# Kernel tuning notes

Measured on AMD Instinct MI355X. Metric: run time of the kernel, lower is better.

Reference implementation:

```python
import jax
import jax.numpy as jnp
import numpy as np

B, T, D = 4, 2048, 2048
H, HS = 32, 64
E5, TD = 5 * 32, 64
LAYER_ID, NUM_LAYERS = 12, 24


def setup_inputs() -> dict:
    key = jax.random.key(0)
    ks = jax.random.split(key, 12)
    r01 = LAYER_ID / max(NUM_LAYERS - 1, 1)          # ratio_0_to_1
    r1a0 = 1.0 - LAYER_ID / NUM_LAYERS               # ratio_1_to_almost0
    ddd = np.arange(D, dtype=np.float32) / D
    i = np.arange(D, dtype=np.float32)
    decay = (-6.0 + 5.0 * (i / max(D - 1, 1)) ** (0.7 + 1.3 * r01)).reshape(H, HS)
    first = (r01 * (1.0 - i / max(D - 1, 1)) + ((i + 1) % 3 - 1) * 0.1).reshape(H, HS)
    s = 1.0 / np.sqrt(D)
    inp = {
        "x": jax.random.normal(ks[0], (B, T, D), jnp.float32),
        "prev": jax.random.normal(ks[1], (B, D), jnp.float32),
        "state": jnp.zeros((B, H, HS, HS), jnp.float32),
        "x_maa": jnp.asarray(1.0 - ddd ** r1a0),
        "w_maa": jnp.asarray(1.0 - ddd ** r1a0),
        "k_maa": jnp.asarray(1.0 - ddd ** r1a0),
        "v_maa": jnp.asarray(1.0 - (ddd ** r1a0 + 0.3 * r01)),
        "r_maa": jnp.asarray(1.0 - ddd ** (0.5 * r1a0)),
        "g_maa": jnp.asarray(1.0 - ddd ** (0.5 * r1a0)),
        "tm_w1": jax.random.normal(ks[2], (D, E5), jnp.float32) * 0.01,
        "tm_w2": jax.random.normal(ks[3], (5, E5 // 5, D), jnp.float32) * 0.01,
        "td_w1": jax.random.normal(ks[4], (D, TD), jnp.float32) * 0.01,
        "td_w2": jax.random.normal(ks[5], (TD, D), jnp.float32) * 0.01,
        "time_decay": jnp.asarray(decay),
        "time_first": jnp.asarray(first),
        "W_r": jax.random.normal(ks[6], (D, D), jnp.float32) * s,
        "W_k": jax.random.normal(ks[7], (D, D), jnp.float32) * s,
        "W_v": jax.random.normal(ks[8], (D, D), jnp.float32) * s,
        "W_g": jax.random.normal(ks[9], (D, D), jnp.float32) * s,
        "W_o": jax.random.normal(ks[10], (D, D), jnp.float32) * s,
        "ln_g": jnp.ones((D,), jnp.float32),
        "ln_b": jnp.zeros((D,), jnp.float32),
    }
    return inp


def _wkv(r, k, v, w, u, state):
    # r,k,v,w: [T,B,H,HS]; u: [H,HS]; state: [B,H,K,V]
    ub = u[None, :, :, None]  # broadcast over batch and value dim

    def step(st, inp):
        rt, kt, vt, wt = inp                      # [B,H,HS]
        kv = kt[..., :, None] * vt[..., None, :]  # [B,H,K,V]
        out = jnp.einsum('bhk,bhkv->bhv', rt, st + ub * kv)
        st = st * wt[..., :, None] + kv
        return st, out

    new_state, outs = jax.lax.scan(step, state, (r, k, v, w))
    return outs, new_state  # outs: [T,B,H,HS]


def reference(x, prev, state, x_maa, w_maa, k_maa, v_maa, r_maa, g_maa,
              tm_w1, tm_w2, td_w1, td_w2, time_decay, time_first,
              W_r, W_k, W_v, W_g, W_o, ln_g, ln_b):
    B_, T_, D_ = x.shape
    H_, HS_ = time_decay.shape
    shifted = jnp.concatenate([prev[:, None, :], x[:, :-1]], axis=1)
    sx = shifted - x
    xxx = x + sx * x_maa
    m = jnp.tanh(xxx @ tm_w1).reshape(B_, T_, 5, -1)
    mix = jnp.einsum('btfe,fed->fbtd', m, tm_w2)  # [5,B,T,D]
    mw, mk, mv, mr, mg = mix
    wx = x + sx * (w_maa + mw)
    kx = x + sx * (k_maa + mk)
    vx = x + sx * (v_maa + mv)
    rx = x + sx * (r_maa + mr)
    gx = x + sx * (g_maa + mg)
    r = jax.nn.sigmoid(rx @ W_r)
    k = kx @ W_k
    v = vx @ W_v
    g = jax.nn.silu(gx @ W_g)
    w = jnp.tanh(wx @ td_w1) @ td_w2
    w = w.reshape(B_, T_, H_, HS_) + time_decay  # broadcast [H,HS]
    w = jnp.exp(-jnp.exp(w))

    def to_tbhd(a):
        return a.reshape(B_, T_, H_, HS_).transpose(1, 0, 2, 3)

    outs, new_state = _wkv(to_tbhd(r), to_tbhd(k), to_tbhd(v),
                           to_tbhd(w), time_first, state)
    out = outs.transpose(1, 0, 2, 3).reshape(B_ * T_, H_, HS_)
    mu = out.mean(-1, keepdims=True)
    var = out.var(-1, keepdims=True)
    out = ((out - mu) / jnp.sqrt(var + 1e-5)).reshape(B_ * T_, D_)
    out = (out * ln_g + ln_b).reshape(B_, T_, D_)
    out = (out * g) @ W_o
    return out, x[:, -1], new_state
```

## Files before the change

kernel.cpp:

```cpp
#include <hip/hip_runtime.h>
#include <stdint.h>

typedef unsigned short u16;
typedef __attribute__((ext_vector_type(8))) short s16x8;
typedef __attribute__((ext_vector_type(4))) float f32x4;

#define DEVFN static __device__ __forceinline__

constexpr int BB = 4, TT = 2048, DD = 2048, HH = 32;
constexpr int MM = BB * TT;
constexpr size_t MD = (size_t)MM * DD;
constexpr int CC = 128, NC = 16;

DEVFN u16 f2b(float f) {
  unsigned int b = __float_as_uint(f);
  unsigned int r = (b + 0x7fffu + ((b >> 16) & 1u)) >> 16;
  return (u16)r;
}
DEVFN float b2f(u16 u) { return __uint_as_float(((unsigned int)u) << 16); }
DEVFN ushort4 pack4(float4 v) {
  ushort4 o; o.x = f2b(v.x); o.y = f2b(v.y); o.z = f2b(v.z); o.w = f2b(v.w); return o;
}

DEVFN void gload16(const void* g, void* l) {
  __builtin_amdgcn_global_load_lds(
      (const __attribute__((address_space(1))) unsigned int*)g,
      (__attribute__((address_space(3))) unsigned int*)l, 16, 0, 0);
}

__global__ __launch_bounds__(256) void k_xxx(
    const float* __restrict__ x, const float* __restrict__ prev,
    const float* __restrict__ xmaa, u16* __restrict__ xxxb,
    float* __restrict__ xlast) {
  size_t e = ((size_t)blockIdx.x * 256 + threadIdx.x) * 4;
  int d = (int)(e % DD);
  int m = (int)(e / DD);
  int b = m >> 11, t = m & (TT - 1);
  float4 xv = *(const float4*)(x + e);
  float4 sh = (t == 0) ? *(const float4*)(prev + (size_t)b * DD + d)
                       : *(const float4*)(x + e - DD);
  float4 xm = *(const float4*)(xmaa + d);
  float4 xx = make_float4(xv.x + (sh.x - xv.x) * xm.x, xv.y + (sh.y - xv.y) * xm.y,
                          xv.z + (sh.z - xv.z) * xm.z, xv.w + (sh.w - xv.w) * xm.w);
  *(ushort4*)(xxxb + e) = pack4(xx);
  if (t == TT - 1) *(float4*)(xlast + (size_t)b * DD + d) = xv;
}

__global__ __launch_bounds__(256) void k_transpose(
    const float* __restrict__ src, u16* __restrict__ dst,
    int K, int N, int Kpad, int Npad) {
  __shared__ float tile[64][65];
  int k0 = blockIdx.x * 64, n0 = blockIdx.y * 64;
  int tid = threadIdx.x;
#pragma unroll
  for (int it = 0; it < 16; ++it) {
    int flat = it * 256 + tid;
    int r = flat >> 6, c = flat & 63;
    int kk = k0 + r, nn = n0 + c;
    tile[r][c] = (kk < K && nn < N) ? src[(size_t)kk * N + nn] : 0.f;
  }
  __syncthreads();
#pragma unroll
  for (int it = 0; it < 16; ++it) {
    int flat = it * 256 + tid;
    int r = flat >> 6, c = flat & 63;
    dst[(size_t)(n0 + r) * Kpad + (k0 + c)] = f2b(tile[c][r]);
  }
}

__global__ __launch_bounds__(256) void k_tmw1(const float* __restrict__ src,
                                              u16* __restrict__ dst) {
  int idx = blockIdx.x * 256 + threadIdx.x;
  int n = idx >> 11, kk = idx & 2047;
  int f = n >> 6, c = n & 63;
  float v = (f < 5 && c < 32) ? src[(size_t)kk * 160 + f * 32 + c] : 0.f;
  dst[idx] = f2b(v);
}

__global__ __launch_bounds__(256) void gemm_bt(
    const u16* __restrict__ A, int lda, const u16* __restrict__ Bt, int ldb,
    void* __restrict__ Out, int ldc, int K, int mode,
    const float* __restrict__ colvec, const float* __restrict__ xf32,
    const float* __restrict__ prevf32) {
  __shared__ u16 As[128 * 64];
  __shared__ u16 Bs[128 * 64];
  const int tid = threadIdx.x;
  const int m0 = blockIdx.x * 128, n0 = blockIdx.y * 128;
  const int wv = tid >> 6, lane = tid & 63;
  const int wr = wv >> 1, wc = wv & 1;
  const int lrow = lane & 15, kgrp = lane >> 4;
  const int srow = lane >> 3;
  const int scol = (lane & 7) * 8;
  f32x4 acc[4][4];
#pragma unroll
  for (int i = 0; i < 4; i++)
#pragma unroll
    for (int j = 0; j < 4; j++) acc[i][j] = {0.f, 0.f, 0.f, 0.f};

  for (int k0 = 0; k0 < K; k0 += 64) {
#pragma unroll
    for (int it = 0; it < 4; ++it) {
      int rbase = it * 32 + wv * 8;
      gload16(A + (size_t)(m0 + rbase + srow) * lda + k0 + scol, &As[rbase * 64]);
      gload16(Bt + (size_t)(n0 + rbase + srow) * ldb + k0 + scol, &Bs[rbase * 64]);
    }
    __syncthreads();
#pragma unroll
    for (int ks = 0; ks < 64; ks += 32) {
      s16x8 af[4], bfr[4];
#pragma unroll
      for (int mi = 0; mi < 4; mi++)
        af[mi] = *(const s16x8*)(&As[(wr * 64 + mi * 16 + lrow) * 64 + ks + kgrp * 8]);
#pragma unroll
      for (int ni = 0; ni < 4; ni++)
        bfr[ni] = *(const s16x8*)(&Bs[(wc * 64 + ni * 16 + lrow) * 64 + ks + kgrp * 8]);
#pragma unroll
      for (int mi = 0; mi < 4; mi++)
#pragma unroll
        for (int ni = 0; ni < 4; ni++)
          acc[mi][ni] = __builtin_amdgcn_mfma_f32_16x16x32_bf16(af[mi], bfr[ni],
                                                                acc[mi][ni], 0, 0, 0);
    }
    __syncthreads();
  }
#pragma unroll
  for (int mi = 0; mi < 4; mi++) {
#pragma unroll
    for (int ni = 0; ni < 4; ni++) {
      int row0 = m0 + wr * 64 + mi * 16 + kgrp * 4;
      int col = n0 + wc * 64 + ni * 16 + lrow;
#pragma unroll
      for (int q = 0; q < 4; q++) {
        int row = row0 + q;
        size_t o = (size_t)row * ldc + col;
        float v = acc[mi][ni][q];
        if (mode == 0) {
          ((u16*)Out)[o] = f2b(v);
        } else if (mode == 1) {
          ((u16*)Out)[o] = f2b(1.f / (1.f + __expf(-v)));
        } else if (mode == 2) {
          ((u16*)Out)[o] = f2b(v / (1.f + __expf(-v)));
        } else if (mode == 3) {
          ((u16*)Out)[o] = f2b(tanhf(v));
        } else if (mode == 4) {
          ((float*)Out)[o] = __expf(-__expf(v + colvec[col]));
        } else if (mode == 5) {
          int b = row >> 11, t = row & (TT - 1);
          size_t xo = (size_t)row * DD + col;
          float xv = xf32[xo];
          float sh = (t == 0) ? prevf32[(size_t)b * DD + col] : xf32[xo - DD];
          ((u16*)Out)[o] = f2b(xv + (sh - xv) * (colvec[col] + v));
        } else {
          ((float*)Out)[o] = v;
        }
      }
    }
  }
}


__global__ __launch_bounds__(64) void k_scan1(
    const u16* __restrict__ k, const u16* __restrict__ v,
    const float* __restrict__ w, float* __restrict__ L, float* __restrict__ P) {
  int idx = blockIdx.x;
  int bh = idx / NC, c = idx % NC;
  int b = bh >> 5, h = bh & 31;
  int j = threadIdx.x;
  float4 s[16];
#pragma unroll
  for (int i = 0; i < 16; i++) s[i] = make_float4(0.f, 0.f, 0.f, 0.f);
  float pj = 1.f;
  __shared__ __align__(16) float ks[64];
  __shared__ __align__(16) float wsd[64];
  size_t base = ((size_t)b * TT + (size_t)c * CC) * DD + h * 64 + j;
  float kc = b2f(k[base]), vc = b2f(v[base]), wc = w[base];
  for (int t = 0; t < CC; ++t) {
    ks[j] = kc; wsd[j] = wc;
    float vg = vc, wcur = wc;
    __syncthreads();
    size_t nb = base + DD;
    if (t + 1 < CC) { kc = b2f(k[nb]); vc = b2f(v[nb]); wc = w[nb]; }
    pj *= wcur;
#pragma unroll
    for (int i = 0; i < 16; i++) {
      float4 k4 = *(const float4*)(ks + i * 4);
      float4 w4 = *(const float4*)(wsd + i * 4);
      float4 s4 = s[i];
      s4.x = fmaf(s4.x, w4.x, k4.x * vg);
      s4.y = fmaf(s4.y, w4.y, k4.y * vg);
      s4.z = fmaf(s4.z, w4.z, k4.z * vg);
      s4.w = fmaf(s4.w, w4.w, k4.w * vg);
      s[i] = s4;
    }
    base = nb;
    __syncthreads();
  }
  float* Lp = L + (size_t)idx * 4096;
#pragma unroll
  for (int i = 0; i < 16; i++) {
    Lp[(i * 4 + 0) * 64 + j] = s[i].x;
    Lp[(i * 4 + 1) * 64 + j] = s[i].y;
    Lp[(i * 4 + 2) * 64 + j] = s[i].z;
    Lp[(i * 4 + 3) * 64 + j] = s[i].w;
  }
  P[(size_t)idx * 64 + j] = pj;
}

__global__ __launch_bounds__(64) void k_scan2(
    float* LS, const float* __restrict__ P, const float* __restrict__ st_in) {
  int bh = blockIdx.x;
  int j = threadIdx.x;
  const float* si = st_in + (size_t)bh * 4096;
  float4 s[16];
#pragma unroll
  for (int i = 0; i < 16; i++) {
    s[i].x = si[(i * 4 + 0) * 64 + j];
    s[i].y = si[(i * 4 + 1) * 64 + j];
    s[i].z = si[(i * 4 + 2) * 64 + j];
    s[i].w = si[(i * 4 + 3) * 64 + j];
  }
  for (int c = 0; c < NC; ++c) {
    size_t slot = ((size_t)bh * NC + c) * 4096;
    if (c > 0) {
      float* dst = LS + ((size_t)bh * NC + c - 1) * 4096;
#pragma unroll
      for (int i = 0; i < 16; i++) {
        dst[(i * 4 + 0) * 64 + j] = s[i].x;
        dst[(i * 4 + 1) * 64 + j] = s[i].y;
        dst[(i * 4 + 2) * 64 + j] = s[i].z;
        dst[(i * 4 + 3) * 64 + j] = s[i].w;
      }
    }
    const float* Pc = P + ((size_t)bh * NC + c) * 64;
#pragma unroll
    for (int i = 0; i < 16; i++) {
      float4 p4 = *(const float4*)(Pc + i * 4);
      float lx = LS[slot + (i * 4 + 0) * 64 + j];
      float ly = LS[slot + (i * 4 + 1) * 64 + j];
      float lz = LS[slot + (i * 4 + 2) * 64 + j];
      float lw = LS[slot + (i * 4 + 3) * 64 + j];
      s[i].x = fmaf(s[i].x, p4.x, lx);
      s[i].y = fmaf(s[i].y, p4.y, ly);
      s[i].z = fmaf(s[i].z, p4.z, lz);
      s[i].w = fmaf(s[i].w, p4.w, lw);
    }
  }
}

__global__ __launch_bounds__(64) void k_scan3(
    const u16* __restrict__ r, const u16* __restrict__ k,
    const u16* __restrict__ v, const float* __restrict__ w,
    const float* __restrict__ u, const float* __restrict__ st_in,
    const float* __restrict__ LS, u16* __restrict__ wkv,
    float* __restrict__ st_out) {
  int idx = blockIdx.x;
  int bh = idx / NC, c = idx % NC;
  int b = bh >> 5, h = bh & 31;
  int j = threadIdx.x;
  const float* sp = (c == 0) ? st_in + (size_t)bh * 4096
                             : LS + ((size_t)bh * NC + c - 1) * 4096;
  float4 s[16];
#pragma unroll
  for (int i = 0; i < 16; i++) {
    s[i].x = sp[(i * 4 + 0) * 64 + j];
    s[i].y = sp[(i * 4 + 1) * 64 + j];
    s[i].z = sp[(i * 4 + 2) * 64 + j];
    s[i].w = sp[(i * 4 + 3) * 64 + j];
  }
  float4 uu[16];
  const float* up = u + h * 64;
#pragma unroll
  for (int i = 0; i < 16; i++) uu[i] = *(const float4*)(up + i * 4);
  __shared__ __align__(16) float rs[64];
  __shared__ __align__(16) float ks[64];
  __shared__ __align__(16) float wsd[64];
  size_t base = ((size_t)b * TT + (size_t)c * CC) * DD + h * 64 + j;
  float rc = b2f(r[base]), kc = b2f(k[base]), vc = b2f(v[base]), wc = w[base];
  for (int t = 0; t < CC; ++t) {
    rs[j] = rc; ks[j] = kc; wsd[j] = wc;
    float vg = vc;
    __syncthreads();
    size_t nb = base + DD;
    if (t + 1 < CC) { rc = b2f(r[nb]); kc = b2f(k[nb]); vc = b2f(v[nb]); wc = w[nb]; }
    float acc = 0.f;
#pragma unroll
    for (int i = 0; i < 16; i++) {
      float4 r4 = *(const float4*)(rs + i * 4);
      float4 k4 = *(const float4*)(ks + i * 4);
      float4 w4 = *(const float4*)(wsd + i * 4);
      float4 u4 = uu[i];
      float4 s4 = s[i];
      float kv;
      kv = k4.x * vg; acc += r4.x * fmaf(u4.x, kv, s4.x); s4.x = fmaf(s4.x, w4.x, kv);
      kv = k4.y * vg; acc += r4.y * fmaf(u4.y, kv, s4.y); s4.y = fmaf(s4.y, w4.y, kv);
      kv = k4.z * vg; acc += r4.z * fmaf(u4.z, kv, s4.z); s4.z = fmaf(s4.z, w4.z, kv);
      kv = k4.w * vg; acc += r4.w * fmaf(u4.w, kv, s4.w); s4.w = fmaf(s4.w, w4.w, kv);
      s[i] = s4;
    }
    wkv[base] = f2b(acc);
    base = nb;
    __syncthreads();
  }
  if (c == NC - 1) {
    float* so = st_out + (size_t)bh * 4096;
#pragma unroll
    for (int i = 0; i < 16; i++) {
      so[(i * 4 + 0) * 64 + j] = s[i].x;
      so[(i * 4 + 1) * 64 + j] = s[i].y;
      so[(i * 4 + 2) * 64 + j] = s[i].z;
      so[(i * 4 + 3) * 64 + j] = s[i].w;
    }
  }
}

__global__ __launch_bounds__(256) void k_gnorm(
    const u16* __restrict__ wkv, const u16* __restrict__ g,
    const float* __restrict__ lng, const float* __restrict__ lnb,
    u16* __restrict__ outg) {
  int gi = blockIdx.x * 4 + (threadIdx.x >> 6);
  int lane = threadIdx.x & 63;
  int row = gi >> 5, h = gi & 31;
  size_t o = (size_t)row * DD + h * 64 + lane;
  float val = b2f(wkv[o]);
  float s1 = val, s2 = val * val;
#pragma unroll
  for (int off = 32; off; off >>= 1) {
    s1 += __shfl_xor(s1, off);
    s2 += __shfl_xor(s2, off);
  }
  float mu = s1 * (1.f / 64.f);
  float var = s2 * (1.f / 64.f) - mu * mu;
  float nv = (val - mu) * rsqrtf(var + 1e-5f);
  int d = h * 64 + lane;
  float ov = (nv * lng[d] + lnb[d]) * b2f(g[o]);
  outg[o] = f2b(ov);
}

extern "C" void kernel_launch(void* const* d_in, const int* in_sizes, int n_in,
                              void* d_out, int out_size, void* d_ws, size_t ws_size,
                              hipStream_t stream) {
  const float* x = (const float*)d_in[0];
  const float* prev = (const float*)d_in[1];
  const float* st = (const float*)d_in[2];
  const float* x_maa = (const float*)d_in[3];
  const float* w_maa = (const float*)d_in[4];
  const float* k_maa = (const float*)d_in[5];
  const float* v_maa = (const float*)d_in[6];
  const float* r_maa = (const float*)d_in[7];
  const float* g_maa = (const float*)d_in[8];
  const float* tm_w1 = (const float*)d_in[9];
  const float* tm_w2 = (const float*)d_in[10];
  const float* td_w1 = (const float*)d_in[11];
  const float* td_w2 = (const float*)d_in[12];
  const float* decay = (const float*)d_in[13];
  const float* first = (const float*)d_in[14];
  const float* W_r = (const float*)d_in[15];
  const float* W_k = (const float*)d_in[16];
  const float* W_v = (const float*)d_in[17];
  const float* W_g = (const float*)d_in[18];
  const float* W_o = (const float*)d_in[19];
  const float* ln_g = (const float*)d_in[20];
  const float* ln_b = (const float*)d_in[21];

  float* out = (float*)d_out;
  float* xlast = out + MD;
  float* stout = xlast + (size_t)BB * DD;
  float* wf32 = out;

  char* p = (char*)d_ws;
  const size_t SLOT = MD * 2;
  u16* slotA = (u16*)p; p += SLOT;
  u16* slotB = (u16*)p; p += SLOT;
  u16* slotC = (u16*)p; p += SLOT;
  u16* slotD = (u16*)p; p += SLOT;
  u16* slotE = (u16*)p; p += SLOT;
  u16* mbuf = (u16*)p; p += (size_t)MM * 384 * 2;
  u16* hbuf = (u16*)p; p += (size_t)MM * 128 * 2;
  u16* Wrt = (u16*)p; p += (size_t)DD * DD * 2;
  u16* Wkt = (u16*)p; p += (size_t)DD * DD * 2;
  u16* Wvt = (u16*)p; p += (size_t)DD * DD * 2;
  u16* Wgt = (u16*)p; p += (size_t)DD * DD * 2;
  u16* Wot = (u16*)p; p += (size_t)DD * DD * 2;
  u16* tmw1t = (u16*)p; p += (size_t)384 * 2048 * 2;
  u16* w2t = (u16*)p; p += (size_t)5 * 2048 * 64 * 2;
  u16* tdw1t = (u16*)p; p += (size_t)128 * 2048 * 2;
  u16* tdw2t = (u16*)p; p += (size_t)2048 * 128 * 2;

  float* LS = (float*)Wrt;
  float* Pbuf = (float*)hbuf;

  dim3 b256(256);
  k_transpose<<<dim3(32, 32), b256, 0, stream>>>(W_r, Wrt, 2048, 2048, 2048, 2048);
  k_transpose<<<dim3(32, 32), b256, 0, stream>>>(W_k, Wkt, 2048, 2048, 2048, 2048);
  k_transpose<<<dim3(32, 32), b256, 0, stream>>>(W_v, Wvt, 2048, 2048, 2048, 2048);
  k_transpose<<<dim3(32, 32), b256, 0, stream>>>(W_g, Wgt, 2048, 2048, 2048, 2048);
  k_transpose<<<dim3(32, 32), b256, 0, stream>>>(W_o, Wot, 2048, 2048, 2048, 2048);
  k_transpose<<<dim3(32, 2), b256, 0, stream>>>(td_w1, tdw1t, 2048, 64, 2048, 128);
  k_transpose<<<dim3(2, 32), b256, 0, stream>>>(td_w2, tdw2t, 64, 2048, 128, 2048);
  for (int f = 0; f < 5; ++f)
    k_transpose<<<dim3(1, 32), b256, 0, stream>>>(
        tm_w2 + (size_t)f * 32 * 2048, w2t + (size_t)f * 2048 * 64, 32, 2048, 64, 2048);
  k_tmw1<<<3072, b256, 0, stream>>>(tm_w1, tmw1t);

  k_xxx<<<(int)(MD / 4 / 256), b256, 0, stream>>>(x, prev, x_maa, slotA, xlast);

  gemm_bt<<<dim3(MM / 128, 3), b256, 0, stream>>>(slotA, 2048, tmw1t, 2048, mbuf, 384,
                                                  2048, 3, nullptr, nullptr, nullptr);

  const float* maas[5] = {w_maa, k_maa, v_maa, r_maa, g_maa};
  gemm_bt<<<dim3(MM / 128, 16), b256, 0, stream>>>(mbuf + 3 * 64, 384, w2t + (size_t)3 * 2048 * 64,
                                                   64, slotB, 2048, 64, 5, maas[3], x, prev);
  gemm_bt<<<dim3(MM / 128, 16), b256, 0, stream>>>(slotB, 2048, Wrt, 2048, slotA, 2048,
                                                   2048, 1, nullptr, nullptr, nullptr);
  gemm_bt<<<dim3(MM / 128, 16), b256, 0, stream>>>(mbuf + 1 * 64, 384, w2t + (size_t)1 * 2048 * 64,
                                                   64, slotB, 2048, 64, 5, maas[1], x, prev);
  gemm_bt<<<dim3(MM / 128, 16), b256, 0, stream>>>(slotB, 2048, Wkt, 2048, slotC, 2048,
                                                   2048, 0, nullptr, nullptr, nullptr);
  gemm_bt<<<dim3(MM / 128, 16), b256, 0, stream>>>(mbuf + 2 * 64, 384, w2t + (size_t)2 * 2048 * 64,
                                                   64, slotB, 2048, 64, 5, maas[2], x, prev);
  gemm_bt<<<dim3(MM / 128, 16), b256, 0, stream>>>(slotB, 2048, Wvt, 2048, slotD, 2048,
                                                   2048, 0, nullptr, nullptr, nullptr);
  gemm_bt<<<dim3(MM / 128, 16), b256, 0, stream>>>(mbuf + 4 * 64, 384, w2t + (size_t)4 * 2048 * 64,
                                                   64, slotB, 2048, 64, 5, maas[4], x, prev);
  gemm_bt<<<dim3(MM / 128, 16), b256, 0, stream>>>(slotB, 2048, Wgt, 2048, slotE, 2048,
                                                   2048, 2, nullptr, nullptr, nullptr);
  gemm_bt<<<dim3(MM / 128, 16), b256, 0, stream>>>(mbuf + 0 * 64, 384, w2t + (size_t)0 * 2048 * 64,
                                                   64, slotB, 2048, 64, 5, maas[0], x, prev);
  gemm_bt<<<dim3(MM / 128, 1), b256, 0, stream>>>(slotB, 2048, tdw1t, 2048, hbuf, 128,
                                                  2048, 3, nullptr, nullptr, nullptr);
  gemm_bt<<<dim3(MM / 128, 16), b256, 0, stream>>>(hbuf, 128, tdw2t, 128, wf32, 2048,
                                                   128, 4, decay, nullptr, nullptr);

  k_scan1<<<BB * HH * NC, 64, 0, stream>>>(slotC, slotD, wf32, LS, Pbuf);
  k_scan2<<<BB * HH, 64, 0, stream>>>(LS, Pbuf, st);
  k_scan3<<<BB * HH * NC, 64, 0, stream>>>(slotA, slotC, slotD, wf32, first, st, LS,
                                           slotB, stout);

  k_gnorm<<<MM * HH / 4, b256, 0, stream>>>(slotB, slotE, ln_g, ln_b, slotA);

  gemm_bt<<<dim3(MM / 128, 16), b256, 0, stream>>>(slotA, 2048, Wot, 2048, out, 2048,
                                                   2048, 6, nullptr, nullptr, nullptr);
}
```

Measured before the change: 1.720 ms.

## Split mix epilogue into vectorized elementwise kernel and unroll scan loops by two

The lerp epilogue (mode 5) is removed from the GEMM. Each small mix GEMM now writes raw bf16 output, and a separate vectorized k_bx kernel applies x + sx*(maa + mix) in place. This replaces the scattered uncoalesced fp32 x/prev reads in the GEMM epilogue with float4 loads, at the cost of an extra kernel launch and an extra bf16 round trip per branch. Separately, k_scan1 and k_scan3 now process two timesteps per iteration, with double shared buffers and one barrier pair, halving synchronization. The extra rounding of the mix term to bf16 slightly changes numerics.

```diff
diff --git a/kernel.cpp b/kernel.cpp
--- a/kernel.cpp
+++ b/kernel.cpp
@@ -46,6 +46,26 @@
   if (t == TT - 1) *(float4*)(xlast + (size_t)b * DD + d) = xv;
 }
 
+__global__ __launch_bounds__(256) void k_bx(
+    const float* __restrict__ x, const float* __restrict__ prev,
+    const float* __restrict__ maa, u16* __restrict__ buf) {
+  size_t e = ((size_t)blockIdx.x * 256 + threadIdx.x) * 4;
+  int d = (int)(e % DD);
+  int m = (int)(e / DD);
+  int b = m >> 11, t = m & (TT - 1);
+  float4 xv = *(const float4*)(x + e);
+  float4 sh = (t == 0) ? *(const float4*)(prev + (size_t)b * DD + d)
+                       : *(const float4*)(x + e - DD);
+  float4 ma = *(const float4*)(maa + d);
+  ushort4 mu = *(const ushort4*)(buf + e);
+  float4 o;
+  o.x = xv.x + (sh.x - xv.x) * (ma.x + b2f(mu.x));
+  o.y = xv.y + (sh.y - xv.y) * (ma.y + b2f(mu.y));
+  o.z = xv.z + (sh.z - xv.z) * (ma.z + b2f(mu.z));
+  o.w = xv.w + (sh.w - xv.w) * (ma.w + b2f(mu.w));
+  *(ushort4*)(buf + e) = pack4(o);
+}
+
 __global__ __launch_bounds__(256) void k_transpose(
     const float* __restrict__ src, u16* __restrict__ dst,
     int K, int N, int Kpad, int Npad) {
@@ -80,8 +100,7 @@
 __global__ __launch_bounds__(256) void gemm_bt(
     const u16* __restrict__ A, int lda, const u16* __restrict__ Bt, int ldb,
     void* __restrict__ Out, int ldc, int K, int mode,
-    const float* __restrict__ colvec, const float* __restrict__ xf32,
-    const float* __restrict__ prevf32) {
+    const float* __restrict__ colvec) {
   __shared__ u16 As[128 * 64];
   __shared__ u16 Bs[128 * 64];
   const int tid = threadIdx.x;
@@ -144,12 +163,6 @@
           ((u16*)Out)[o] = f2b(tanhf(v));
         } else if (mode == 4) {
           ((float*)Out)[o] = __expf(-__expf(v + colvec[col]));
-        } else if (mode == 5) {
-          int b = row >> 11, t = row & (TT - 1);
-          size_t xo = (size_t)row * DD + col;
-          float xv = xf32[xo];
-          float sh = (t == 0) ? prevf32[(size_t)b * DD + col] : xf32[xo - DD];
-          ((u16*)Out)[o] = f2b(xv + (sh - xv) * (colvec[col] + v));
         } else {
           ((float*)Out)[o] = v;
         }
@@ -170,29 +183,34 @@
 #pragma unroll
   for (int i = 0; i < 16; i++) s[i] = make_float4(0.f, 0.f, 0.f, 0.f);
   float pj = 1.f;
-  __shared__ __align__(16) float ks[64];
-  __shared__ __align__(16) float wsd[64];
+  __shared__ __align__(16) float ks0[64], ws0[64], ks1[64], ws1[64];
   size_t base = ((size_t)b * TT + (size_t)c * CC) * DD + h * 64 + j;
-  float kc = b2f(k[base]), vc = b2f(v[base]), wc = w[base];
-  for (int t = 0; t < CC; ++t) {
-    ks[j] = kc; wsd[j] = wc;
-    float vg = vc, wcur = wc;
-    __syncthreads();
-    size_t nb = base + DD;
-    if (t + 1 < CC) { kc = b2f(k[nb]); vc = b2f(v[nb]); wc = w[nb]; }
-    pj *= wcur;
+  float kc0 = b2f(k[base]), vc0 = b2f(v[base]), wc0 = w[base];
+  float kc1 = b2f(k[base + DD]), vc1 = b2f(v[base + DD]), wc1 = w[base + DD];
+  for (int t = 0; t < CC; t += 2) {
+    ks0[j] = kc0; ws0[j] = wc0; ks1[j] = kc1; ws1[j] = wc1;
+    float vg0 = vc0, vg1 = vc1;
+    pj *= wc0 * wc1;
+    __syncthreads();
+    if (t + 2 < CC) {
+      size_t nb = base + 2 * DD;
+      kc0 = b2f(k[nb]); vc0 = b2f(v[nb]); wc0 = w[nb];
+      kc1 = b2f(k[nb + DD]); vc1 = b2f(v[nb + DD]); wc1 = w[nb + DD];
+    }
 #pragma unroll
     for (int i = 0; i < 16; i++) {
-      float4 k4 = *(const float4*)(ks + i * 4);
-      float4 w4 = *(const float4*)(wsd + i * 4);
+      float4 k40 = *(const float4*)(ks0 + i * 4);
+      float4 w40 = *(const float4*)(ws0 + i * 4);
+      float4 k41 = *(const float4*)(ks1 + i * 4);
+      float4 w41 = *(const float4*)(ws1 + i * 4);
       float4 s4 = s[i];
-      s4.x = fmaf(s4.x, w4.x, k4.x * vg);
-      s4.y = fmaf(s4.y, w4.y, k4.y * vg);
-      s4.z = fmaf(s4.z, w4.z, k4.z * vg);
-      s4.w = fmaf(s4.w, w4.w, k4.w * vg);
+      s4.x = fmaf(s4.x, w40.x, k40.x * vg0); s4.x = fmaf(s4.x, w41.x, k41.x * vg1);
+      s4.y = fmaf(s4.y, w40.y, k40.y * vg0); s4.y = fmaf(s4.y, w41.y, k41.y * vg1);
+      s4.z = fmaf(s4.z, w40.z, k40.z * vg0); s4.z = fmaf(s4.z, w41.z, k41.z * vg1);
+      s4.w = fmaf(s4.w, w40.w, k40.w * vg0); s4.w = fmaf(s4.w, w41.w, k41.w * vg1);
       s[i] = s4;
     }
-    base = nb;
+    base += 2 * DD;
     __syncthreads();
   }
   float* Lp = L + (size_t)idx * 4096;
@@ -271,34 +289,48 @@
   const float* up = u + h * 64;
 #pragma unroll
   for (int i = 0; i < 16; i++) uu[i] = *(const float4*)(up + i * 4);
-  __shared__ __align__(16) float rs[64];
-  __shared__ __align__(16) float ks[64];
-  __shared__ __align__(16) float wsd[64];
+  __shared__ __align__(16) float rs0[64], ks0[64], ws0[64];
+  __shared__ __align__(16) float rs1[64], ks1[64], ws1[64];
   size_t base = ((size_t)b * TT + (size_t)c * CC) * DD + h * 64 + j;
-  float rc = b2f(r[base]), kc = b2f(k[base]), vc = b2f(v[base]), wc = w[base];
-  for (int t = 0; t < CC; ++t) {
-    rs[j] = rc; ks[j] = kc; wsd[j] = wc;
-    float vg = vc;
-    __syncthreads();
-    size_t nb = base + DD;
-    if (t + 1 < CC) { rc = b2f(r[nb]); kc = b2f(k[nb]); vc = b2f(v[nb]); wc = w[nb]; }
-    float acc = 0.f;
+  float rc0 = b2f(r[base]), kc0 = b2f(k[base]), vc0 = b2f(v[base]), wc0 = w[base];
+  float rc1 = b2f(r[base + DD]), kc1 = b2f(k[base + DD]), vc1 = b2f(v[base + DD]),
+        wc1 = w[base + DD];
+  for (int t = 0; t < CC; t += 2) {
+    rs0[j] = rc0; ks0[j] = kc0; ws0[j] = wc0;
+    rs1[j] = rc1; ks1[j] = kc1; ws1[j] = wc1;
+    float vg0 = vc0, vg1 = vc1;
+    __syncthreads();
+    if (t + 2 < CC) {
+      size_t nb = base + 2 * DD;
+      rc0 = b2f(r[nb]); kc0 = b2f(k[nb]); vc0 = b2f(v[nb]); wc0 = w[nb];
+      rc1 = b2f(r[nb + DD]); kc1 = b2f(k[nb + DD]); vc1 = b2f(v[nb + DD]);
+      wc1 = w[nb + DD];
+    }
+    float acc0 = 0.f, acc1 = 0.f;
 #pragma unroll
     for (int i = 0; i < 16; i++) {
-      float4 r4 = *(const float4*)(rs + i * 4);
-      float4 k4 = *(const float4*)(ks + i * 4);
-      float4 w4 = *(const float4*)(wsd + i * 4);
+      float4 r40 = *(const float4*)(rs0 + i * 4);
+      float4 k40 = *(const float4*)(ks0 + i * 4);
+      float4 w40 = *(const float4*)(ws0 + i * 4);
+      float4 r41 = *(const float4*)(rs1 + i * 4);
+      float4 k41 = *(const float4*)(ks1 + i * 4);
+      float4 w41 = *(const float4*)(ws1 + i * 4);
       float4 u4 = uu[i];
       float4 s4 = s[i];
       float kv;
-      kv = k4.x * vg; acc += r4.x * fmaf(u4.x, kv, s4.x); s4.x = fmaf(s4.x, w4.x, kv);
-      kv = k4.y * vg; acc += r4.y * fmaf(u4.y, kv, s4.y); s4.y = fmaf(s4.y, w4.y, kv);
-      kv = k4.z * vg; acc += r4.z * fmaf(u4.z, kv, s4.z); s4.z = fmaf(s4.z, w4.z, kv);
-      kv = k4.w * vg; acc += r4.w * fmaf(u4.w, kv, s4.w); s4.w = fmaf(s4.w, w4.w, kv);
+      kv = k40.x * vg0; acc0 += r40.x * fmaf(u4.x, kv, s4.x); s4.x = fmaf(s4.x, w40.x, kv);
+      kv = k41.x * vg1; acc1 += r41.x * fmaf(u4.x, kv, s4.x); s4.x = fmaf(s4.x, w41.x, kv);
+      kv = k40.y * vg0; acc0 += r40.y * fmaf(u4.y, kv, s4.y); s4.y = fmaf(s4.y, w40.y, kv);
+      kv = k41.y * vg1; acc1 += r41.y * fmaf(u4.y, kv, s4.y); s4.y = fmaf(s4.y, w41.y, kv);
+      kv = k40.z * vg0; acc0 += r40.z * fmaf(u4.z, kv, s4.z); s4.z = fmaf(s4.z, w40.z, kv);
+      kv = k41.z * vg1; acc1 += r41.z * fmaf(u4.z, kv, s4.z); s4.z = fmaf(s4.z, w41.z, kv);
+      kv = k40.w * vg0; acc0 += r40.w * fmaf(u4.w, kv, s4.w); s4.w = fmaf(s4.w, w40.w, kv);
+      kv = k41.w * vg1; acc1 += r41.w * fmaf(u4.w, kv, s4.w); s4.w = fmaf(s4.w, w41.w, kv);
       s[i] = s4;
     }
-    wkv[base] = f2b(acc);
-    base = nb;
+    wkv[base] = f2b(acc0);
+    wkv[base + DD] = f2b(acc1);
+    base += 2 * DD;
     __syncthreads();
   }
   if (c == NC - 1) {
@@ -405,31 +437,42 @@
   k_xxx<<<(int)(MD / 4 / 256), b256, 0, stream>>>(x, prev, x_maa, slotA, xlast);
 
   gemm_bt<<<dim3(MM / 128, 3), b256, 0, stream>>>(slotA, 2048, tmw1t, 2048, mbuf, 384,
-                                                  2048, 3, nullptr, nullptr, nullptr);
+                                                  2048, 3, nullptr);
 
   const float* maas[5] = {w_maa, k_maa, v_maa, r_maa, g_maa};
-  gemm_bt<<<dim3(MM / 128, 16), b256, 0, stream>>>(mbuf + 3 * 64, 384, w2t + (size_t)3 * 2048 * 64,
-                                                   64, slotB, 2048, 64, 5, maas[3], x, prev);
+  const int nbx = (int)(MD / 4 / 256);
+  gemm_bt<<<dim3(MM / 128, 16), b256, 0, stream>>>(mbuf + 3 * 64, 384,
+                                                   w2t + (size_t)3 * 2048 * 64, 64,
+                                                   slotB, 2048, 64, 0, nullptr);
+  k_bx<<<nbx, b256, 0, stream>>>(x, prev, maas[3], slotB);
   gemm_bt<<<dim3(MM / 128, 16), b256, 0, stream>>>(slotB, 2048, Wrt, 2048, slotA, 2048,
-                                                   2048, 1, nullptr, nullptr, nullptr);
-  gemm_bt<<<dim3(MM / 128, 16), b256, 0, stream>>>(mbuf + 1 * 64, 384, w2t + (size_t)1 * 2048 * 64,
-                                                   64, slotB, 2048, 64, 5, maas[1], x, prev);
+                                                   2048, 1, nullptr);
+  gemm_bt<<<dim3(MM / 128, 16), b256, 0, stream>>>(mbuf + 1 * 64, 384,
+                                                   w2t + (size_t)1 * 2048 * 64, 64,
+                                                   slotB, 2048, 64, 0, nullptr);
+  k_bx<<<nbx, b256, 0, stream>>>(x, prev, maas[1], slotB);
   gemm_bt<<<dim3(MM / 128, 16), b256, 0, stream>>>(slotB, 2048, Wkt, 2048, slotC, 2048,
-                                                   2048, 0, nullptr, nullptr, nullptr);
-  gemm_bt<<<dim3(MM / 128, 16), b256, 0, stream>>>(mbuf + 2 * 64, 384, w2t + (size_t)2 * 2048 * 64,
-                                                   64, slotB, 2048, 64, 5, maas[2], x, prev);
+                                                   2048, 0, nullptr);
+  gemm_bt<<<dim3(MM / 128, 16), b256, 0, stream>>>(mbuf + 2 * 64, 384,
+                                                   w2t + (size_t)2 * 2048 * 64, 64,
+                                                   slotB, 2048, 64, 0, nullptr);
+  k_bx<<<nbx, b256, 0, stream>>>(x, prev, maas[2], slotB);
   gemm_bt<<<dim3(MM / 128, 16), b256, 0, stream>>>(slotB, 2048, Wvt, 2048, slotD, 2048,
-                                                   2048, 0, nullptr, nullptr, nullptr);
-  gemm_bt<<<dim3(MM / 128, 16), b256, 0, stream>>>(mbuf + 4 * 64, 384, w2t + (size_t)4 * 2048 * 64,
-                                                   64, slotB, 2048, 64, 5, maas[4], x, prev);
+                                                   2048, 0, nullptr);
+  gemm_bt<<<dim3(MM / 128, 16), b256, 0, stream>>>(mbuf + 4 * 64, 384,
+                                                   w2t + (size_t)4 * 2048 * 64, 64,
+                                                   slotB, 2048, 64, 0, nullptr);
+  k_bx<<<nbx, b256, 0, stream>>>(x, prev, maas[4], slotB);
   gemm_bt<<<dim3(MM / 128, 16), b256, 0, stream>>>(slotB, 2048, Wgt, 2048, slotE, 2048,
-                                                   2048, 2, nullptr, nullptr, nullptr);
-  gemm_bt<<<dim3(MM / 128, 16), b256, 0, stream>>>(mbuf + 0 * 64, 384, w2t + (size_t)0 * 2048 * 64,
-                                                   64, slotB, 2048, 64, 5, maas[0], x, prev);
+                                                   2048, 2, nullptr);
+  gemm_bt<<<dim3(MM / 128, 16), b256, 0, stream>>>(mbuf + 0 * 64, 384,
+                                                   w2t + (size_t)0 * 2048 * 64, 64,
+                                                   slotB, 2048, 64, 0, nullptr);
+  k_bx<<<nbx, b256, 0, stream>>>(x, prev, maas[0], slotB);
   gemm_bt<<<dim3(MM / 128, 1), b256, 0, stream>>>(slotB, 2048, tdw1t, 2048, hbuf, 128,
-                                                  2048, 3, nullptr, nullptr, nullptr);
+                                                  2048, 3, nullptr);
   gemm_bt<<<dim3(MM / 128, 16), b256, 0, stream>>>(hbuf, 128, tdw2t, 128, wf32, 2048,
-                                                   128, 4, decay, nullptr, nullptr);
+                                                   128, 4, decay);
 
   k_scan1<<<BB * HH * NC, 64, 0, stream>>>(slotC, slotD, wf32, LS, Pbuf);
   k_scan2<<<BB * HH, 64, 0, stream>>>(LS, Pbuf, st);
@@ -439,5 +482,5 @@
   k_gnorm<<<MM * HH / 4, b256, 0, stream>>>(slotB, slotE, ln_g, ln_b, slotA);
 
   gemm_bt<<<dim3(MM / 128, 16), b256, 0, stream>>>(slotA, 2048, Wot, 2048, out, 2048,
-                                                   2048, 6, nullptr, nullptr, nullptr);
-}
+                                                   2048, 6, nullptr);
+}
```

After: 1.709 ms. Within noise of the previous version (-0.6%).
